# Kernel tuning notes

Measured on AMD Instinct MI355X. Metric: run time of the kernel, lower is better.

Reference implementation:

```python
import jax, jax.numpy as jnp
import numpy as np

EMBED_DIM = 1024
NUM_HEADS = 16
HEAD_DIM = EMBED_DIM // NUM_HEADS
ROPE_BASE = 10000.0


def _rope_cos_sin(seq_len, head_dim, dtype):
    # Standard RoPE (ESM-style rotate_half): freqs outer(t, inv_freq), emb = cat(freqs, freqs)
    inv_freq = 1.0 / (ROPE_BASE ** (jnp.arange(0, head_dim, 2, dtype=jnp.float32) / head_dim))
    t = jnp.arange(seq_len, dtype=jnp.float32)
    freqs = jnp.einsum('s,d->sd', t, inv_freq)          # [s, d/2]
    emb = jnp.concatenate([freqs, freqs], axis=-1)      # [s, d]
    return jnp.cos(emb).astype(dtype), jnp.sin(emb).astype(dtype)


def _rotate_half(x):
    x1, x2 = jnp.split(x, 2, axis=-1)
    return jnp.concatenate([-x2, x1], axis=-1)


def _apply_rope(x, cos, sin):
    # x: [b, h, s, d]; cos/sin: [s, d] broadcast over b, h
    return x * cos + _rotate_half(x) * sin


def setup_inputs() -> dict:
    key = jax.random.key(0)
    ks = jax.random.split(key, 5)
    b, s, e = 4, 2048, EMBED_DIM
    scale = 1.0 / np.sqrt(e)
    x = jax.random.normal(ks[0], (b, s, e), dtype=jnp.float32)
    Wqkv = jax.random.normal(ks[1], (e, 3 * e), dtype=jnp.float32) * scale
    bqkv = jnp.zeros((3 * e,), dtype=jnp.float32)
    Wo = jax.random.normal(ks[2], (e, e), dtype=jnp.float32) * scale
    bo = jnp.zeros((e,), dtype=jnp.float32)
    return {"x": x, "Wqkv": Wqkv, "bqkv": bqkv, "Wo": Wo, "bo": bo}


def reference(x, Wqkv, bqkv, Wo, bo):
    b, s, e = x.shape
    h, d = NUM_HEADS, HEAD_DIM
    qkv = jnp.einsum('bse,ef->bsf', x, Wqkv) + bqkv          # [b, s, 3e]
    q, k, v = jnp.split(qkv, 3, axis=-1)
    # b s (h d) -> b h s d
    q = q.reshape(b, s, h, d).transpose(0, 2, 1, 3)
    k = k.reshape(b, s, h, d).transpose(0, 2, 1, 3)
    v = v.reshape(b, s, h, d).transpose(0, 2, 1, 3)
    cos, sin = _rope_cos_sin(s, d, x.dtype)
    q = _apply_rope(q, cos, sin)
    k = _apply_rope(k, cos, sin)
    # scaled dot product attention (no mask, no dropout, non-causal)
    scores = jnp.einsum('bhqd,bhkd->bhqk', q, k) / jnp.asarray(np.sqrt(d), x.dtype)
    attn = jax.nn.softmax(scores, axis=-1)
    out = jnp.einsum('bhqk,bhkd->bhqd', attn, v)             # [b, h, s, d]
    out = out.transpose(0, 2, 1, 3).reshape(b, s, e)         # b h s d -> b s (h d)
    return jnp.einsum('bse,ef->bsf', out, Wo) + bo
```

## Files before the change

kernel.cpp:

```cpp
#include <hip/hip_runtime.h>
#include <stdint.h>
#include <stddef.h>

typedef __bf16 bf16;
typedef __attribute__((ext_vector_type(8))) __bf16 bf16x8;
typedef __attribute__((ext_vector_type(4))) __bf16 bf16x4;
typedef __attribute__((ext_vector_type(4))) float f32x4;
typedef __attribute__((ext_vector_type(16))) float f32x16;
typedef __attribute__((ext_vector_type(4))) float float4v;
typedef __attribute__((ext_vector_type(4))) uint32_t u32x4;

#define BATCH 4
#define SEQ   2048
#define EMB   1024
#define NH    16
#define HD    64
#define F3    3072

#define MFMA16(a, b, c) __builtin_amdgcn_mfma_f32_16x16x32_bf16((a), (b), (c), 0, 0, 0)
#define MFMA32(a, b, c) __builtin_amdgcn_mfma_f32_32x32x16_bf16((a), (b), (c), 0, 0, 0)

__device__ __forceinline__ void gload_lds16(const bf16* g, bf16* l) {
  __builtin_amdgcn_global_load_lds(
      (const __attribute__((address_space(1))) uint32_t*)g,
      (__attribute__((address_space(3))) uint32_t*)l, 16, 0, 0);
}

__device__ __forceinline__ int mod10(int x) { return x >= 10 ? x - 10 : x; }

__device__ __forceinline__ void transpose_tile32(const float* __restrict__ in,
                                                 bf16* __restrict__ out,
                                                 int R, int C, int bx, int by) {
  __shared__ bf16 tile[32][33];
  const int tx = threadIdx.x & 31;
  const int ty = threadIdx.x >> 5;
  const int c0 = bx * 32, r0 = by * 32;
#pragma unroll
  for (int kk = 0; kk < 4; ++kk) {
    int r = ty + kk * 8;
    tile[r][tx] = (bf16)in[(size_t)(r0 + r) * C + c0 + tx];
  }
  __syncthreads();
#pragma unroll
  for (int kk = 0; kk < 4; ++kk) {
    int r = ty + kk * 8;
    out[(size_t)(c0 + r) * R + r0 + tx] = tile[tx][r];
  }
}

__global__ __launch_bounds__(256) void prep_kernel(const float* __restrict__ x_raw,
                                                   bf16* __restrict__ xb,
                                                   const float* __restrict__ wqkv_raw,
                                                   bf16* __restrict__ wqkvT,
                                                   float* __restrict__ cosT,
                                                   float* __restrict__ sinT) {
  const int blk = blockIdx.x;
  if (blk < 8192) {
    int i = blk * 256 + threadIdx.x;
    float4v v = ((const float4v*)x_raw)[i];
    bf16x4 o;
#pragma unroll
    for (int k = 0; k < 4; ++k) o[k] = (bf16)v[k];
    ((bf16x4*)xb)[i] = o;
  } else if (blk < 11264) {
    int idx = blk - 8192;
    transpose_tile32(wqkv_raw, wqkvT, EMB, F3, idx % 96, idx / 96);
  } else {
    int idx = (blk - 11264) * 256 + threadIdx.x;
    int pos = idx >> 5, d1 = idx & 31;
    float inv = powf(10000.0f, -(float)(2 * d1) / 64.0f);
    float th = (float)pos * inv;
    cosT[idx] = cosf(th);
    sinT[idx] = sinf(th);
  }
}

__global__ __launch_bounds__(256) void transpose_f32_bf16(const float* __restrict__ in,
                                                          bf16* __restrict__ out,
                                                          int R, int C) {
  transpose_tile32(in, out, R, C, blockIdx.x, blockIdx.y);
}

__device__ __forceinline__ void gemm256_core(bf16* lds,
                                             const bf16* __restrict__ Abase,
                                             const bf16* __restrict__ Bbase,
                                             f32x4 (&acc)[8][4]) {
  const int tid = threadIdx.x;
  const int w = tid >> 6, lane = tid & 63;
  const int lhi = lane >> 4, llo = lane & 15, l7 = llo & 7;
  const int wr = w >> 2, wc = w & 3;
  const int srow = lane >> 3;
  const int sk16 = (lane & 7) ^ srow;
  const size_t g_lane = (size_t)(w * 16 + srow) * EMB + sk16 * 8;
  bf16* ldsw = lds + w * 1024;

  const int ka0 = (lhi * 8) ^ (l7 << 3);
  const int ka1 = (32 + lhi * 8) ^ (l7 << 3);
  const int arow = llo * 64;
  const int brow = ((wc & 1) * 64 + llo) * 64;

#pragma unroll
  for (int i = 0; i < 8; ++i)
#pragma unroll
    for (int j = 0; j < 4; ++j) acc[i][j] = (f32x4){0.f, 0.f, 0.f, 0.f};

#define STAGE(baseptr, slot)                              \
  do {                                                    \
    const bf16* _b = (baseptr);                           \
    bf16* _l = ldsw + (slot) * 8192;                      \
    gload_lds16(_b + g_lane, _l);                         \
    gload_lds16(_b + g_lane + 8 * EMB, _l + 512);         \
  } while (0)

  STAGE(Abase, 0);
  STAGE(Abase + 128 * EMB, 1);
  STAGE(Bbase, 2);
  STAGE(Bbase + 128 * EMB, 3);
  STAGE(Abase + 64, 4);
  STAGE(Abase + 128 * EMB + 64, 5);
  asm volatile("s_waitcnt vmcnt(4)" ::: "memory");
  __builtin_amdgcn_s_barrier();

  int rs = 0;
#pragma unroll 1
  for (int t = 0; t < 16; ++t) {
    const bf16* ldsA = lds + mod10(rs + wr) * 8192 + arow;
    const bf16* ldsB = lds + mod10(rs + 2 + (wc >> 1)) * 8192 + brow;
    const int k1 = (t + 1) * 64;
    const int k2 = (t + 2) * 64;
    bf16x8 a[4][2], b0[2][2], b1[2][2];

#pragma unroll
    for (int i = 0; i < 4; ++i) {
      a[i][0] = *(const bf16x8*)(ldsA + i * 1024 + ka0);
      a[i][1] = *(const bf16x8*)(ldsA + i * 1024 + ka1);
    }
#pragma unroll
    for (int j = 0; j < 2; ++j) {
      b0[j][0] = *(const bf16x8*)(ldsB + j * 1024 + ka0);
      b0[j][1] = *(const bf16x8*)(ldsB + j * 1024 + ka1);
    }
    if (t < 15) STAGE(Bbase + k1, mod10(rs + 6));
    __builtin_amdgcn_s_barrier();
    asm volatile("s_waitcnt lgkmcnt(0)" ::: "memory");
    __builtin_amdgcn_sched_barrier(0);
    __builtin_amdgcn_s_setprio(1);
#pragma unroll
    for (int i = 0; i < 4; ++i)
#pragma unroll
      for (int j = 0; j < 2; ++j) {
        acc[i][j] = MFMA16(a[i][0], b0[j][0], acc[i][j]);
        acc[i][j] = MFMA16(a[i][1], b0[j][1], acc[i][j]);
      }
    __builtin_amdgcn_s_setprio(0);
    __builtin_amdgcn_s_barrier();

#pragma unroll
    for (int j = 0; j < 2; ++j) {
      b1[j][0] = *(const bf16x8*)(ldsB + 2048 + j * 1024 + ka0);
      b1[j][1] = *(const bf16x8*)(ldsB + 2048 + j * 1024 + ka1);
    }
    if (t < 15) STAGE(Bbase + 128 * EMB + k1, mod10(rs + 7));
    __builtin_amdgcn_s_barrier();
    asm volatile("s_waitcnt lgkmcnt(0)" ::: "memory");
    __builtin_amdgcn_sched_barrier(0);
    __builtin_amdgcn_s_setprio(1);
#pragma unroll
    for (int i = 0; i < 4; ++i)
#pragma unroll
      for (int j = 0; j < 2; ++j) {
        acc[i][2 + j] = MFMA16(a[i][0], b1[j][0], acc[i][2 + j]);
        acc[i][2 + j] = MFMA16(a[i][1], b1[j][1], acc[i][2 + j]);
      }
    __builtin_amdgcn_s_setprio(0);
    __builtin_amdgcn_s_barrier();

#pragma unroll
    for (int i = 0; i < 4; ++i) {
      a[i][0] = *(const bf16x8*)(ldsA + 4096 + i * 1024 + ka0);
      a[i][1] = *(const bf16x8*)(ldsA + 4096 + i * 1024 + ka1);
    }
    if (t < 14) STAGE(Abase + k2, mod10(rs + 8));
    __builtin_amdgcn_s_barrier();
    asm volatile("s_waitcnt lgkmcnt(0)" ::: "memory");
    __builtin_amdgcn_sched_barrier(0);
    __builtin_amdgcn_s_setprio(1);
#pragma unroll
    for (int i = 0; i < 4; ++i)
#pragma unroll
      for (int j = 0; j < 2; ++j) {
        acc[4 + i][2 + j] = MFMA16(a[i][0], b1[j][0], acc[4 + i][2 + j]);
        acc[4 + i][2 + j] = MFMA16(a[i][1], b1[j][1], acc[4 + i][2 + j]);
      }
    __builtin_amdgcn_s_setprio(0);
    __builtin_amdgcn_s_barrier();

    if (t < 14) STAGE(Abase + 128 * EMB + k2, mod10(rs + 9));
    __builtin_amdgcn_s_barrier();
    asm volatile("s_waitcnt lgkmcnt(0)" ::: "memory");
    __builtin_amdgcn_sched_barrier(0);
    __builtin_amdgcn_s_setprio(1);
#pragma unroll
    for (int i = 0; i < 4; ++i)
#pragma unroll
      for (int j = 0; j < 2; ++j) {
        acc[4 + i][j] = MFMA16(a[i][0], b0[j][0], acc[4 + i][j]);
        acc[4 + i][j] = MFMA16(a[i][1], b0[j][1], acc[4 + i][j]);
      }
    __builtin_amdgcn_s_setprio(0);
    if (t < 14) {
      asm volatile("s_waitcnt vmcnt(4)" ::: "memory");
    } else if (t == 14) {
      asm volatile("s_waitcnt vmcnt(0)" ::: "memory");
    }
    if (t < 15) __builtin_amdgcn_s_barrier();

    rs += 4;
    if (rs >= 10) rs -= 10;
  }
#undef STAGE
}

__global__ __launch_bounds__(512, 2) void qkv8_kernel(
    const bf16* __restrict__ x, const bf16* __restrict__ wT,
    const float* __restrict__ bias, bf16* __restrict__ qo, bf16* __restrict__ ko,
    bf16* __restrict__ vo, const float* __restrict__ cosT,
    const float* __restrict__ sinT) {
  extern __shared__ __align__(16) bf16 ldsb[];
  const int orig = blockIdx.x;
  const int wg = (orig & 7) * 48 + (orig >> 3);
  const int bx = wg % 12, by = wg / 12;
  const int row_a0 = by * 256, row_b0 = bx * 256;

  f32x4 acc[8][4];
  gemm256_core(ldsb, x + (size_t)row_a0 * EMB, wT + (size_t)row_b0 * EMB, acc);

  const int tid = threadIdx.x;
  const int w = tid >> 6, lane = tid & 63;
  const int lhi = lane >> 4, llo = lane & 15;
  const int wr = w >> 2, wc = w & 3;

  const int f0 = row_b0 + wc * 64;
  const int part = f0 >> 10;
  const int hh = (f0 & 1023) >> 6;
  const int m_base = row_a0 + wr * 128;

  float bvals[4];
#pragma unroll
  for (int j = 0; j < 4; ++j) bvals[j] = bias[f0 + j * 16 + llo];

  if (part == 2) {
#pragma unroll
    for (int mi = 0; mi < 8; ++mi) {
      int m0 = m_base + mi * 16 + lhi * 4;
      int bb = m0 >> 11, pos0 = m0 & 2047;
#pragma unroll
      for (int j = 0; j < 4; ++j) {
        int dd = j * 16 + llo;
        bf16x4 pk;
#pragma unroll
        for (int r = 0; r < 4; ++r) pk[r] = (bf16)(acc[mi][j][r] + bvals[j]);
        *(bf16x4*)(vo + ((size_t)(bb * NH + hh) * HD + dd) * SEQ + pos0) = pk;
      }
    }
  } else {
    bf16* dst = (part == 0) ? qo : ko;
    const float qs = (part == 0) ? 0.125f : 1.0f;
#pragma unroll
    for (int mi = 0; mi < 8; ++mi) {
#pragma unroll
      for (int r = 0; r < 4; ++r) {
        int m = m_base + mi * 16 + lhi * 4 + r;
        int bb = m >> 11, pos = m & 2047;
        size_t base = ((size_t)(bb * NH + hh) * SEQ + pos) * HD;
#pragma unroll
        for (int j = 0; j < 2; ++j) {
          int d1 = j * 16 + llo;
          float x1 = acc[mi][j][r] + bvals[j];
          float x2 = acc[mi][j + 2][r] + bvals[j + 2];
          float cth = cosT[pos * 32 + d1];
          float sth = sinT[pos * 32 + d1];
          dst[base + d1] = (bf16)((x1 * cth - x2 * sth) * qs);
          dst[base + d1 + 32] = (bf16)((x2 * cth + x1 * sth) * qs);
        }
      }
    }
  }
}

__global__ __launch_bounds__(512, 2) void outproj8_kernel(
    const bf16* __restrict__ a_in, const bf16* __restrict__ wT,
    const float* __restrict__ bo, float* __restrict__ out) {
  extern __shared__ __align__(16) bf16 ldsb[];
  const int orig = blockIdx.x;
  const int wg = (orig & 7) * 16 + (orig >> 3);
  const int bx = wg % 4, by = wg / 4;
  const int row_a0 = by * 256, row_b0 = bx * 256;

  f32x4 acc[8][4];
  gemm256_core(ldsb, a_in + (size_t)row_a0 * EMB, wT + (size_t)row_b0 * EMB, acc);

  const int tid = threadIdx.x;
  const int w = tid >> 6, lane = tid & 63;
  const int lhi = lane >> 4, llo = lane & 15;
  const int wr = w >> 2, wc = w & 3;

  const int col0 = row_b0 + wc * 64;
  const int m_base = row_a0 + wr * 128;
  float bvals[4];
#pragma unroll
  for (int j = 0; j < 4; ++j) bvals[j] = bo[col0 + j * 16 + llo];
#pragma unroll
  for (int mi = 0; mi < 8; ++mi) {
#pragma unroll
    for (int r = 0; r < 4; ++r) {
      int m = m_base + mi * 16 + lhi * 4 + r;
#pragma unroll
      for (int j = 0; j < 4; ++j)
        out[(size_t)m * EMB + col0 + j * 16 + llo] = acc[mi][j][r] + bvals[j];
    }
  }
}

__global__ __launch_bounds__(512, 2) void attn32_kernel(const bf16* __restrict__ q,
                                                        const bf16* __restrict__ k,
                                                        const bf16* __restrict__ vT,
                                                        bf16* __restrict__ o) {
  __shared__ __align__(16) bf16 smem[16384];

  const int tid = threadIdx.x, w = tid >> 6, lane = tid & 63;
  const int l31 = lane & 31, hi = lane >> 5;
  const int bidx = blockIdx.x;
  const int vblk = (bidx & 7) * 64 + (bidx >> 3);
  const int qt = vblk & 7, bh = vblk >> 3;
  const bf16* qbase = q + (size_t)bh * SEQ * HD + qt * 256 * HD;
  const bf16* kbase = k + (size_t)bh * SEQ * HD;
  const bf16* vbase = vT + (size_t)bh * HD * SEQ;

  const int rowc = lane >> 3;
  const int sw8 = (lane & 7) ^ rowc;

  bf16x8 qf[4];
  {
    const bf16* qrow = qbase + (size_t)(w * 32 + l31) * HD;
#pragma unroll
    for (int c = 0; c < 4; ++c) qf[c] = *(const bf16x8*)(qrow + c * 16 + hi * 8);
  }

  if (w < 4) {
#pragma unroll
    for (int c = 0; c < 2; ++c) {
      int ch = w * 2 + c, row = ch * 8 + rowc;
      gload_lds16(kbase + (size_t)row * HD + sw8 * 8, &smem[ch * 512]);
    }
  } else {
#pragma unroll
    for (int c = 0; c < 2; ++c) {
      int ch = (w - 4) * 2 + c, row = ch * 8 + rowc;
      gload_lds16(vbase + (size_t)row * SEQ + sw8 * 8, &smem[8192 + ch * 512]);
    }
  }
  __syncthreads();

  float rsum = 0.f;
  f32x16 oacc[2];
#pragma unroll
  for (int r = 0; r < 16; ++r) { oacc[0][r] = 0.f; oacc[1][r] = 0.f; }

  const int swz = (l31 & 7);

  for (int kb = 0; kb < 32; ++kb) {
    bf16* Kc = smem + (kb & 1) * 4096;
    bf16* Vc = smem + 8192 + (kb & 1) * 4096;
    if (kb < 31) {
      int kpos = (kb + 1) * 64;
      if (w < 4) {
        bf16* Kn = smem + ((kb + 1) & 1) * 4096;
#pragma unroll
        for (int c = 0; c < 2; ++c) {
          int ch = w * 2 + c, row = ch * 8 + rowc;
          gload_lds16(kbase + (size_t)(kpos + row) * HD + sw8 * 8, &Kn[ch * 512]);
        }
      } else {
        bf16* Vn = smem + 8192 + ((kb + 1) & 1) * 4096;
#pragma unroll
        for (int c = 0; c < 2; ++c) {
          int ch = (w - 4) * 2 + c, row = ch * 8 + rowc;
          gload_lds16(vbase + (size_t)row * SEQ + kpos + sw8 * 8, &Vn[ch * 512]);
        }
      }
    }

    f32x16 st0, st1;
#pragma unroll
    for (int r = 0; r < 16; ++r) { st0[r] = 0.f; st1[r] = 0.f; }
    __builtin_amdgcn_s_setprio(1);
#pragma unroll
    for (int c = 0; c < 4; ++c) {
      bf16x8 kf0 = *(const bf16x8*)&Kc[l31 * 64 + (((c * 2 + hi) ^ swz) * 8)];
      bf16x8 kf1 = *(const bf16x8*)&Kc[(32 + l31) * 64 + (((c * 2 + hi) ^ swz) * 8)];
      st0 = MFMA32(kf0, qf[c], st0);
      st1 = MFMA32(kf1, qf[c], st1);
    }
    __builtin_amdgcn_s_setprio(0);

#pragma unroll
    for (int r = 0; r < 16; ++r) {
      st0[r] = __expf(st0[r]);
      st1[r] = __expf(st1[r]);
    }
    {
      float a0 = 0.f, a1 = 0.f, a2 = 0.f, a3 = 0.f;
#pragma unroll
      for (int r = 0; r < 16; r += 4) {
        a0 += st0[r];     a1 += st0[r + 1];
        a2 += st0[r + 2]; a3 += st0[r + 3];
      }
#pragma unroll
      for (int r = 0; r < 16; r += 4) {
        a0 += st1[r];     a1 += st1[r + 1];
        a2 += st1[r + 2]; a3 += st1[r + 3];
      }
      rsum += (a0 + a1) + (a2 + a3);
    }

    bf16x8 pa[4];
#pragma unroll
    for (int tt = 0; tt < 2; ++tt) {
#pragma unroll
      for (int c1 = 0; c1 < 2; ++c1) {
        float s0 = tt ? st1[c1 * 8 + 0] : st0[c1 * 8 + 0];
        float s1 = tt ? st1[c1 * 8 + 1] : st0[c1 * 8 + 1];
        float s2 = tt ? st1[c1 * 8 + 2] : st0[c1 * 8 + 2];
        float s3 = tt ? st1[c1 * 8 + 3] : st0[c1 * 8 + 3];
        float s4 = tt ? st1[c1 * 8 + 4] : st0[c1 * 8 + 4];
        float s5 = tt ? st1[c1 * 8 + 5] : st0[c1 * 8 + 5];
        float s6 = tt ? st1[c1 * 8 + 6] : st0[c1 * 8 + 6];
        float s7 = tt ? st1[c1 * 8 + 7] : st0[c1 * 8 + 7];
        uint32_t a0, a1, b0, b1;
        asm("v_cvt_pk_bf16_f32 %0, %1, %2" : "=v"(a0) : "v"(s0), "v"(s1));
        asm("v_cvt_pk_bf16_f32 %0, %1, %2" : "=v"(a1) : "v"(s2), "v"(s3));
        asm("v_cvt_pk_bf16_f32 %0, %1, %2" : "=v"(b0) : "v"(s4), "v"(s5));
        asm("v_cvt_pk_bf16_f32 %0, %1, %2" : "=v"(b1) : "v"(s6), "v"(s7));
        asm("v_permlane32_swap_b32 %0, %1" : "+v"(a0), "+v"(b0));
        asm("v_permlane32_swap_b32 %0, %1" : "+v"(a1), "+v"(b1));
        u32x4 uv = {a0, a1, b0, b1};
        pa[tt * 2 + c1] = __builtin_bit_cast(bf16x8, uv);
      }
    }

    __builtin_amdgcn_s_setprio(1);
#pragma unroll
    for (int c = 0; c < 4; ++c) {
      bf16x8 v0 = *(const bf16x8*)&Vc[l31 * 64 + (((c * 2 + hi) ^ swz) * 8)];
      bf16x8 v1 = *(const bf16x8*)&Vc[(32 + l31) * 64 + (((c * 2 + hi) ^ swz) * 8)];
      oacc[0] = MFMA32(pa[c], v0, oacc[0]);
      oacc[1] = MFMA32(pa[c], v1, oacc[1]);
    }
    __builtin_amdgcn_s_setprio(0);

    __syncthreads();
  }

  rsum += __shfl_xor(rsum, 32);
  const int bb = bh >> 4, hh = bh & 15;
#pragma unroll
  for (int r = 0; r < 16; ++r) {
    int qrow = (r & 3) + 8 * (r >> 2) + 4 * hi;
    float inv = 1.0f / __shfl(rsum, qrow);
    int pos = qt * 256 + w * 32 + qrow;
    size_t base = ((size_t)bb * SEQ + pos) * EMB + hh * HD;
    o[base + l31] = (bf16)(oacc[0][r] * inv);
    o[base + 32 + l31] = (bf16)(oacc[1][r] * inv);
  }
}

extern "C" void kernel_launch(void* const* d_in, const int* in_sizes, int n_in,
                              void* d_out, int out_size, void* d_ws, size_t ws_size,
                              hipStream_t stream) {
  const float* x_raw = (const float*)d_in[0];
  const float* wqkv_raw = (const float*)d_in[1];
  const float* bqkv = (const float*)d_in[2];
  const float* wo_raw = (const float*)d_in[3];
  const float* bo = (const float*)d_in[4];
  float* out = (float*)d_out;

  char* ws = (char*)d_ws;
  bf16* qw = (bf16*)(ws);
  bf16* kw = (bf16*)(ws + 16777216);
  bf16* vw = (bf16*)(ws + 33554432);
  bf16* wqkvT = (bf16*)(ws + 50331648);
  float* cosT = (float*)(ws + 56623104);
  float* sinT = (float*)(ws + 56885248);
  bf16* ow = (bf16*)(ws + 50331648);
  bf16* woT = (bf16*)(ws);
  bf16* xb = (bf16*)d_out;

  static bool attr_set = false;
  if (!attr_set) {
    (void)hipFuncSetAttribute((const void*)qkv8_kernel,
                              hipFuncAttributeMaxDynamicSharedMemorySize, 163840);
    (void)hipFuncSetAttribute((const void*)outproj8_kernel,
                              hipFuncAttributeMaxDynamicSharedMemorySize, 163840);
    attr_set = true;
  }

  prep_kernel<<<11520, 256, 0, stream>>>(x_raw, xb, wqkv_raw, wqkvT, cosT, sinT);

  qkv8_kernel<<<dim3((BATCH * SEQ / 256) * (F3 / 256)), 512, 163840, stream>>>(
      xb, wqkvT, bqkv, qw, kw, vw, cosT, sinT);
  attn32_kernel<<<dim3(BATCH * NH * (SEQ / 256)), 512, 0, stream>>>(qw, kw, vw, ow);

  transpose_f32_bf16<<<dim3(EMB / 32, EMB / 32), 256, 0, stream>>>(wo_raw, woT, EMB, EMB);
  outproj8_kernel<<<dim3((BATCH * SEQ / 256) * (EMB / 256)), 512, 163840, stream>>>(
      ow, woT, bo, out);
}
```

Baseline: 287.2 us.

## Shrink GEMM tiles to 128x256 with a 9-slot LDS ring pipeline

Reworks the shared GEMM core from 256x256 to 128x256 output tiles for both the QKV and output projections. The LDS staging ring shrinks from 10 to 9 slots, and A and B chunks are prefetched two k-steps ahead with a matching vmcnt wait. This doubles the workgroup count, giving better CU occupancy and wave balance on the outproj GEMM, which previously had only 128 blocks. The cost is less operand reuse per tile and more global and LDS traffic per FLOP.

Result: faster. 275.0 us (-4.3%).

```diff
diff --git a/kernel.cpp b/kernel.cpp
--- a/kernel.cpp
+++ b/kernel.cpp
@@ -25,8 +25,6 @@
       (const __attribute__((address_space(1))) uint32_t*)g,
       (__attribute__((address_space(3))) uint32_t*)l, 16, 0, 0);
 }
-
-__device__ __forceinline__ int mod10(int x) { return x >= 10 ? x - 10 : x; }
 
 __device__ __forceinline__ void transpose_tile32(const float* __restrict__ in,
                                                  bf16* __restrict__ out,
@@ -81,13 +79,13 @@
   transpose_tile32(in, out, R, C, blockIdx.x, blockIdx.y);
 }
 
-__device__ __forceinline__ void gemm256_core(bf16* lds,
+__device__ __forceinline__ void gemm128_core(bf16* lds,
                                              const bf16* __restrict__ Abase,
                                              const bf16* __restrict__ Bbase,
-                                             f32x4 (&acc)[8][4]) {
+                                             f32x4 (&acc)[4][4]) {
   const int tid = threadIdx.x;
   const int w = tid >> 6, lane = tid & 63;
-  const int lhi = lane >> 4, llo = lane & 15, l7 = llo & 7;
+  const int lhi = lane >> 4, llo = lane & 15, l7 = llo & 15 & 7;
   const int wr = w >> 2, wc = w & 3;
   const int srow = lane >> 3;
   const int sk16 = (lane & 7) ^ srow;
@@ -96,11 +94,12 @@
 
   const int ka0 = (lhi * 8) ^ (l7 << 3);
   const int ka1 = (32 + lhi * 8) ^ (l7 << 3);
-  const int arow = llo * 64;
+  const int arow = (wr * 64 + llo) * 64;
   const int brow = ((wc & 1) * 64 + llo) * 64;
-
-#pragma unroll
-  for (int i = 0; i < 8; ++i)
+  const int bsel = wc >> 1;
+
+#pragma unroll
+  for (int i = 0; i < 4; ++i)
 #pragma unroll
     for (int j = 0; j < 4; ++j) acc[i][j] = (f32x4){0.f, 0.f, 0.f, 0.f};
 
@@ -113,21 +112,22 @@
   } while (0)
 
   STAGE(Abase, 0);
-  STAGE(Abase + 128 * EMB, 1);
-  STAGE(Bbase, 2);
-  STAGE(Bbase + 128 * EMB, 3);
-  STAGE(Abase + 64, 4);
-  STAGE(Abase + 128 * EMB + 64, 5);
-  asm volatile("s_waitcnt vmcnt(4)" ::: "memory");
+  STAGE(Bbase, 1);
+  STAGE(Bbase + 128 * EMB, 2);
+  STAGE(Abase + 64, 3);
+  STAGE(Bbase + 64, 4);
+  STAGE(Bbase + 128 * EMB + 64, 5);
+  asm volatile("s_waitcnt vmcnt(6)" ::: "memory");
   __builtin_amdgcn_s_barrier();
 
-  int rs = 0;
+  int s = 0;
 #pragma unroll 1
   for (int t = 0; t < 16; ++t) {
-    const bf16* ldsA = lds + mod10(rs + wr) * 8192 + arow;
-    const bf16* ldsB = lds + mod10(rs + 2 + (wc >> 1)) * 8192 + brow;
-    const int k1 = (t + 1) * 64;
+    const bf16* ldsA = lds + s * 8192 + arow;
+    const bf16* ldsB = lds + (s + 1 + bsel) * 8192 + brow;
     const int k2 = (t + 2) * 64;
+    int st2 = s + 6;
+    if (st2 >= 9) st2 -= 9;
     bf16x8 a[4][2], b0[2][2], b1[2][2];
 
 #pragma unroll
@@ -140,7 +140,10 @@
       b0[j][0] = *(const bf16x8*)(ldsB + j * 1024 + ka0);
       b0[j][1] = *(const bf16x8*)(ldsB + j * 1024 + ka1);
     }
-    if (t < 15) STAGE(Bbase + k1, mod10(rs + 6));
+    if (t < 14) {
+      STAGE(Abase + k2, st2);
+      STAGE(Bbase + k2, st2 + 1);
+    }
     __builtin_amdgcn_s_barrier();
     asm volatile("s_waitcnt lgkmcnt(0)" ::: "memory");
     __builtin_amdgcn_sched_barrier(0);
@@ -160,7 +163,7 @@
       b1[j][0] = *(const bf16x8*)(ldsB + 2048 + j * 1024 + ka0);
       b1[j][1] = *(const bf16x8*)(ldsB + 2048 + j * 1024 + ka1);
     }
-    if (t < 15) STAGE(Bbase + 128 * EMB + k1, mod10(rs + 7));
+    if (t < 14) STAGE(Bbase + 128 * EMB + k2, st2 + 2);
     __builtin_amdgcn_s_barrier();
     asm volatile("s_waitcnt lgkmcnt(0)" ::: "memory");
     __builtin_amdgcn_sched_barrier(0);
@@ -173,67 +176,32 @@
         acc[i][2 + j] = MFMA16(a[i][1], b1[j][1], acc[i][2 + j]);
       }
     __builtin_amdgcn_s_setprio(0);
-    __builtin_amdgcn_s_barrier();
-
-#pragma unroll
-    for (int i = 0; i < 4; ++i) {
-      a[i][0] = *(const bf16x8*)(ldsA + 4096 + i * 1024 + ka0);
-      a[i][1] = *(const bf16x8*)(ldsA + 4096 + i * 1024 + ka1);
-    }
-    if (t < 14) STAGE(Abase + k2, mod10(rs + 8));
-    __builtin_amdgcn_s_barrier();
-    asm volatile("s_waitcnt lgkmcnt(0)" ::: "memory");
-    __builtin_amdgcn_sched_barrier(0);
-    __builtin_amdgcn_s_setprio(1);
-#pragma unroll
-    for (int i = 0; i < 4; ++i)
-#pragma unroll
-      for (int j = 0; j < 2; ++j) {
-        acc[4 + i][2 + j] = MFMA16(a[i][0], b1[j][0], acc[4 + i][2 + j]);
-        acc[4 + i][2 + j] = MFMA16(a[i][1], b1[j][1], acc[4 + i][2 + j]);
-      }
-    __builtin_amdgcn_s_setprio(0);
-    __builtin_amdgcn_s_barrier();
-
-    if (t < 14) STAGE(Abase + 128 * EMB + k2, mod10(rs + 9));
-    __builtin_amdgcn_s_barrier();
-    asm volatile("s_waitcnt lgkmcnt(0)" ::: "memory");
-    __builtin_amdgcn_sched_barrier(0);
-    __builtin_amdgcn_s_setprio(1);
-#pragma unroll
-    for (int i = 0; i < 4; ++i)
-#pragma unroll
-      for (int j = 0; j < 2; ++j) {
-        acc[4 + i][j] = MFMA16(a[i][0], b0[j][0], acc[4 + i][j]);
-        acc[4 + i][j] = MFMA16(a[i][1], b0[j][1], acc[4 + i][j]);
-      }
-    __builtin_amdgcn_s_setprio(0);
     if (t < 14) {
-      asm volatile("s_waitcnt vmcnt(4)" ::: "memory");
+      asm volatile("s_waitcnt vmcnt(6)" ::: "memory");
     } else if (t == 14) {
       asm volatile("s_waitcnt vmcnt(0)" ::: "memory");
     }
     if (t < 15) __builtin_amdgcn_s_barrier();
 
-    rs += 4;
-    if (rs >= 10) rs -= 10;
+    s += 3;
+    if (s >= 9) s -= 9;
   }
 #undef STAGE
 }
 
-__global__ __launch_bounds__(512, 2) void qkv8_kernel(
+__global__ __launch_bounds__(512, 2) void qkv128_kernel(
     const bf16* __restrict__ x, const bf16* __restrict__ wT,
     const float* __restrict__ bias, bf16* __restrict__ qo, bf16* __restrict__ ko,
     bf16* __restrict__ vo, const float* __restrict__ cosT,
     const float* __restrict__ sinT) {
   extern __shared__ __align__(16) bf16 ldsb[];
   const int orig = blockIdx.x;
-  const int wg = (orig & 7) * 48 + (orig >> 3);
+  const int wg = (orig & 7) * 96 + (orig >> 3);
   const int bx = wg % 12, by = wg / 12;
-  const int row_a0 = by * 256, row_b0 = bx * 256;
-
-  f32x4 acc[8][4];
-  gemm256_core(ldsb, x + (size_t)row_a0 * EMB, wT + (size_t)row_b0 * EMB, acc);
+  const int row_a0 = by * 128, row_b0 = bx * 256;
+
+  f32x4 acc[4][4];
+  gemm128_core(ldsb, x + (size_t)row_a0 * EMB, wT + (size_t)row_b0 * EMB, acc);
 
   const int tid = threadIdx.x;
   const int w = tid >> 6, lane = tid & 63;
@@ -243,7 +211,7 @@
   const int f0 = row_b0 + wc * 64;
   const int part = f0 >> 10;
   const int hh = (f0 & 1023) >> 6;
-  const int m_base = row_a0 + wr * 128;
+  const int m_base = row_a0 + wr * 64;
 
   float bvals[4];
 #pragma unroll
@@ -251,7 +219,7 @@
 
   if (part == 2) {
 #pragma unroll
-    for (int mi = 0; mi < 8; ++mi) {
+    for (int mi = 0; mi < 4; ++mi) {
       int m0 = m_base + mi * 16 + lhi * 4;
       int bb = m0 >> 11, pos0 = m0 & 2047;
 #pragma unroll
@@ -267,7 +235,7 @@
     bf16* dst = (part == 0) ? qo : ko;
     const float qs = (part == 0) ? 0.125f : 1.0f;
 #pragma unroll
-    for (int mi = 0; mi < 8; ++mi) {
+    for (int mi = 0; mi < 4; ++mi) {
 #pragma unroll
       for (int r = 0; r < 4; ++r) {
         int m = m_base + mi * 16 + lhi * 4 + r;
@@ -288,17 +256,17 @@
   }
 }
 
-__global__ __launch_bounds__(512, 2) void outproj8_kernel(
+__global__ __launch_bounds__(512, 2) void outproj128_kernel(
     const bf16* __restrict__ a_in, const bf16* __restrict__ wT,
     const float* __restrict__ bo, float* __restrict__ out) {
   extern __shared__ __align__(16) bf16 ldsb[];
   const int orig = blockIdx.x;
-  const int wg = (orig & 7) * 16 + (orig >> 3);
+  const int wg = (orig & 7) * 32 + (orig >> 3);
   const int bx = wg % 4, by = wg / 4;
-  const int row_a0 = by * 256, row_b0 = bx * 256;
-
-  f32x4 acc[8][4];
-  gemm256_core(ldsb, a_in + (size_t)row_a0 * EMB, wT + (size_t)row_b0 * EMB, acc);
+  const int row_a0 = by * 128, row_b0 = bx * 256;
+
+  f32x4 acc[4][4];
+  gemm128_core(ldsb, a_in + (size_t)row_a0 * EMB, wT + (size_t)row_b0 * EMB, acc);
 
   const int tid = threadIdx.x;
   const int w = tid >> 6, lane = tid & 63;
@@ -306,12 +274,12 @@
   const int wr = w >> 2, wc = w & 3;
 
   const int col0 = row_b0 + wc * 64;
-  const int m_base = row_a0 + wr * 128;
+  const int m_base = row_a0 + wr * 64;
   float bvals[4];
 #pragma unroll
   for (int j = 0; j < 4; ++j) bvals[j] = bo[col0 + j * 16 + llo];
 #pragma unroll
-  for (int mi = 0; mi < 8; ++mi) {
+  for (int mi = 0; mi < 4; ++mi) {
 #pragma unroll
     for (int r = 0; r < 4; ++r) {
       int m = m_base + mi * 16 + lhi * 4 + r;
@@ -498,20 +466,20 @@
 
   static bool attr_set = false;
   if (!attr_set) {
-    (void)hipFuncSetAttribute((const void*)qkv8_kernel,
+    (void)hipFuncSetAttribute((const void*)qkv128_kernel,
                               hipFuncAttributeMaxDynamicSharedMemorySize, 163840);
-    (void)hipFuncSetAttribute((const void*)outproj8_kernel,
+    (void)hipFuncSetAttribute((const void*)outproj128_kernel,
                               hipFuncAttributeMaxDynamicSharedMemorySize, 163840);
     attr_set = true;
   }
 
   prep_kernel<<<11520, 256, 0, stream>>>(x_raw, xb, wqkv_raw, wqkvT, cosT, sinT);
 
-  qkv8_kernel<<<dim3((BATCH * SEQ / 256) * (F3 / 256)), 512, 163840, stream>>>(
+  qkv128_kernel<<<dim3((BATCH * SEQ / 128) * (F3 / 256)), 512, 147456, stream>>>(
       xb, wqkvT, bqkv, qw, kw, vw, cosT, sinT);
   attn32_kernel<<<dim3(BATCH * NH * (SEQ / 256)), 512, 0, stream>>>(qw, kw, vw, ow);
 
   transpose_f32_bf16<<<dim3(EMB / 32, EMB / 32), 256, 0, stream>>>(wo_raw, woT, EMB, EMB);
-  outproj8_kernel<<<dim3((BATCH * SEQ / 256) * (EMB / 256)), 512, 163840, stream>>>(
+  outproj128_kernel<<<dim3((BATCH * SEQ / 128) * (EMB / 256)), 512, 147456, stream>>>(
       ow, woT, bo, out);
 }
```

## Use 128x256 tiles with a new pipelined GEMM core for output projection

Applied to the files above, without the earlier changes.

Adds a gemm128_core with 128-row A tiles and a 9-slot LDS ring buffer, and switches the output projection to 128x256 tiles. This doubles the grid from 128 to 256 workgroups so the 256 CUs stay busy, since 128 blocks previously left half the device idle. Each block now does less reuse per tile and needs extra barriers per k-step, and the output projection is only one stage of the pipeline.

Measured after the change: 277.6 us. 1.03x faster.

```diff
diff --git a/kernel.cpp b/kernel.cpp
--- a/kernel.cpp
+++ b/kernel.cpp
@@ -288,17 +288,127 @@
   }
 }
 
-__global__ __launch_bounds__(512, 2) void outproj8_kernel(
+__device__ __forceinline__ void gemm128_core(bf16* lds,
+                                             const bf16* __restrict__ Abase,
+                                             const bf16* __restrict__ Bbase,
+                                             f32x4 (&acc)[4][4]) {
+  const int tid = threadIdx.x;
+  const int w = tid >> 6, lane = tid & 63;
+  const int lhi = lane >> 4, llo = lane & 15, l7 = llo & 15 & 7;
+  const int wr = w >> 2, wc = w & 3;
+  const int srow = lane >> 3;
+  const int sk16 = (lane & 7) ^ srow;
+  const size_t g_lane = (size_t)(w * 16 + srow) * EMB + sk16 * 8;
+  bf16* ldsw = lds + w * 1024;
+
+  const int ka0 = (lhi * 8) ^ (l7 << 3);
+  const int ka1 = (32 + lhi * 8) ^ (l7 << 3);
+  const int arow = (wr * 64 + llo) * 64;
+  const int brow = ((wc & 1) * 64 + llo) * 64;
+  const int bsel = wc >> 1;
+
+#pragma unroll
+  for (int i = 0; i < 4; ++i)
+#pragma unroll
+    for (int j = 0; j < 4; ++j) acc[i][j] = (f32x4){0.f, 0.f, 0.f, 0.f};
+
+#define STAGE(baseptr, slot)                              \
+  do {                                                    \
+    const bf16* _b = (baseptr);                           \
+    bf16* _l = ldsw + (slot) * 8192;                      \
+    gload_lds16(_b + g_lane, _l);                         \
+    gload_lds16(_b + g_lane + 8 * EMB, _l + 512);         \
+  } while (0)
+
+  STAGE(Abase, 0);
+  STAGE(Bbase, 1);
+  STAGE(Bbase + 128 * EMB, 2);
+  STAGE(Abase + 64, 3);
+  STAGE(Bbase + 64, 4);
+  STAGE(Bbase + 128 * EMB + 64, 5);
+  asm volatile("s_waitcnt vmcnt(6)" ::: "memory");
+  __builtin_amdgcn_s_barrier();
+
+  int s = 0;
+#pragma unroll 1
+  for (int t = 0; t < 16; ++t) {
+    const bf16* ldsA = lds + s * 8192 + arow;
+    const bf16* ldsB = lds + (s + 1 + bsel) * 8192 + brow;
+    const int k2 = (t + 2) * 64;
+    int st2 = s + 6;
+    if (st2 >= 9) st2 -= 9;
+    bf16x8 a[4][2], b0[2][2], b1[2][2];
+
+#pragma unroll
+    for (int i = 0; i < 4; ++i) {
+      a[i][0] = *(const bf16x8*)(ldsA + i * 1024 + ka0);
+      a[i][1] = *(const bf16x8*)(ldsA + i * 1024 + ka1);
+    }
+#pragma unroll
+    for (int j = 0; j < 2; ++j) {
+      b0[j][0] = *(const bf16x8*)(ldsB + j * 1024 + ka0);
+      b0[j][1] = *(const bf16x8*)(ldsB + j * 1024 + ka1);
+    }
+    if (t < 14) {
+      STAGE(Abase + k2, st2);
+      STAGE(Bbase + k2, st2 + 1);
+    }
+    __builtin_amdgcn_s_barrier();
+    asm volatile("s_waitcnt lgkmcnt(0)" ::: "memory");
+    __builtin_amdgcn_sched_barrier(0);
+    __builtin_amdgcn_s_setprio(1);
+#pragma unroll
+    for (int i = 0; i < 4; ++i)
+#pragma unroll
+      for (int j = 0; j < 2; ++j) {
+        acc[i][j] = MFMA16(a[i][0], b0[j][0], acc[i][j]);
+        acc[i][j] = MFMA16(a[i][1], b0[j][1], acc[i][j]);
+      }
+    __builtin_amdgcn_s_setprio(0);
+    __builtin_amdgcn_s_barrier();
+
+#pragma unroll
+    for (int j = 0; j < 2; ++j) {
+      b1[j][0] = *(const bf16x8*)(ldsB + 2048 + j * 1024 + ka0);
+      b1[j][1] = *(const bf16x8*)(ldsB + 2048 + j * 1024 + ka1);
+    }
+    if (t < 14) STAGE(Bbase + 128 * EMB + k2, st2 + 2);
+    __builtin_amdgcn_s_barrier();
+    asm volatile("s_waitcnt lgkmcnt(0)" ::: "memory");
+    __builtin_amdgcn_sched_barrier(0);
+    __builtin_amdgcn_s_setprio(1);
+#pragma unroll
+    for (int i = 0; i < 4; ++i)
+#pragma unroll
+      for (int j = 0; j < 2; ++j) {
+        acc[i][2 + j] = MFMA16(a[i][0], b1[j][0], acc[i][2 + j]);
+        acc[i][2 + j] = MFMA16(a[i][1], b1[j][1], acc[i][2 + j]);
+      }
+    __builtin_amdgcn_s_setprio(0);
+    if (t < 14) {
+      asm volatile("s_waitcnt vmcnt(6)" ::: "memory");
+    } else if (t == 14) {
+      asm volatile("s_waitcnt vmcnt(0)" ::: "memory");
+    }
+    if (t < 15) __builtin_amdgcn_s_barrier();
+
+    s += 3;
+    if (s >= 9) s -= 9;
+  }
+#undef STAGE
+}
+
+__global__ __launch_bounds__(512, 2) void outproj128_kernel(
     const bf16* __restrict__ a_in, const bf16* __restrict__ wT,
     const float* __restrict__ bo, float* __restrict__ out) {
   extern __shared__ __align__(16) bf16 ldsb[];
   const int orig = blockIdx.x;
-  const int wg = (orig & 7) * 16 + (orig >> 3);
+  const int wg = (orig & 7) * 32 + (orig >> 3);
   const int bx = wg % 4, by = wg / 4;
-  const int row_a0 = by * 256, row_b0 = bx * 256;
-
-  f32x4 acc[8][4];
-  gemm256_core(ldsb, a_in + (size_t)row_a0 * EMB, wT + (size_t)row_b0 * EMB, acc);
+  const int row_a0 = by * 128, row_b0 = bx * 256;
+
+  f32x4 acc[4][4];
+  gemm128_core(ldsb, a_in + (size_t)row_a0 * EMB, wT + (size_t)row_b0 * EMB, acc);
 
   const int tid = threadIdx.x;
   const int w = tid >> 6, lane = tid & 63;
@@ -306,12 +416,12 @@
   const int wr = w >> 2, wc = w & 3;
 
   const int col0 = row_b0 + wc * 64;
-  const int m_base = row_a0 + wr * 128;
+  const int m_base = row_a0 + wr * 64;
   float bvals[4];
 #pragma unroll
   for (int j = 0; j < 4; ++j) bvals[j] = bo[col0 + j * 16 + llo];
 #pragma unroll
-  for (int mi = 0; mi < 8; ++mi) {
+  for (int mi = 0; mi < 4; ++mi) {
 #pragma unroll
     for (int r = 0; r < 4; ++r) {
       int m = m_base + mi * 16 + lhi * 4 + r;
@@ -500,7 +610,7 @@
   if (!attr_set) {
     (void)hipFuncSetAttribute((const void*)qkv8_kernel,
                               hipFuncAttributeMaxDynamicSharedMemorySize, 163840);
-    (void)hipFuncSetAttribute((const void*)outproj8_kernel,
+    (void)hipFuncSetAttribute((const void*)outproj128_kernel,
                               hipFuncAttributeMaxDynamicSharedMemorySize, 163840);
     attr_set = true;
   }
@@ -512,6 +622,6 @@
   attn32_kernel<<<dim3(BATCH * NH * (SEQ / 256)), 512, 0, stream>>>(qw, kw, vw, ow);
 
   transpose_f32_bf16<<<dim3(EMB / 32, EMB / 32), 256, 0, stream>>>(wo_raw, woT, EMB, EMB);
-  outproj8_kernel<<<dim3((BATCH * SEQ / 256) * (EMB / 256)), 512, 163840, stream>>>(
+  outproj128_kernel<<<dim3((BATCH * SEQ / 128) * (EMB / 256)), 512, 147456, stream>>>(
       ow, woT, bo, out);
 }
```
